# Optimization experiments

Hardware: AMD Instinct MI355X
Metric: run time of the kernel (lower is better)

The kernel has to match this reference:

```python
import jax, jax.numpy as jnp
import numpy as np

L, B, S, D, H, F, V = 6, 4, 512, 768, 12, 3072, 30522
DH = D // H
EPS = 1e-12
SCALE = 1.0 / float(np.sqrt(DH))


def _ln(x, g, b):
    m = jnp.mean(x, axis=-1, keepdims=True)
    v = jnp.mean(jnp.square(x - m), axis=-1, keepdims=True)
    return (x - m) * jax.lax.rsqrt(v + EPS) * g + b


def _mha(xq, xkv, Wq, bq, Wk, bk, Wv, bv, causal):
    Bc, Sq, _ = xq.shape
    Sk = xkv.shape[1]
    q = (xq @ Wq + bq).reshape(Bc, Sq, H, DH).transpose(0, 2, 1, 3)
    k = (xkv @ Wk + bk).reshape(Bc, Sk, H, DH).transpose(0, 2, 1, 3)
    v = (xkv @ Wv + bv).reshape(Bc, Sk, H, DH).transpose(0, 2, 1, 3)
    s = jnp.einsum('bhqd,bhkd->bhqk', q, k) * SCALE
    if causal is not None:
        s = jnp.where(causal[None, None], s, -jnp.inf)
    p = jax.nn.softmax(s, axis=-1)
    ctx = jnp.einsum('bhqk,bhkd->bhqd', p, v)
    return ctx.transpose(0, 2, 1, 3).reshape(Bc, Sq, H * DH)


def _fwd(input_ids, encoder_hidden, word_emb, pos_emb, tok_emb, emb_g, emb_b,
         Wq, bq, Wk, bk, Wv, bv, Wo, bo, ln1_g, ln1_b,
         cWq, cbq, cWk, cbk, cWv, cbv, cWo, cbo, ln2_g, ln2_b,
         Wi, bi, Wf, bf, ln3_g, ln3_b,
         Wt, bt, lnh_g, lnh_b, Wdec, bdec):
    Bc, Sc = input_ids.shape
    # BertEmbeddings: word + position + token_type(all zeros) -> LayerNorm
    h = word_emb[input_ids] + pos_emb[:Sc][None] + tok_emb[0][None, None]
    h = _ln(h, emb_g, emb_b)
    causal = jnp.tril(jnp.ones((Sc, Sc), dtype=bool))
    for l in range(L):
        # causal self-attention + residual LayerNorm
        ctx = _mha(h, h, Wq[l], bq[l], Wk[l], bk[l], Wv[l], bv[l], causal)
        h = _ln(h + ctx @ Wo[l] + bo[l], ln1_g[l], ln1_b[l])
        # cross-attention over encoder_hidden (no mask) + residual LayerNorm
        ctx = _mha(h, encoder_hidden, cWq[l], cbq[l], cWk[l], cbk[l], cWv[l], cbv[l], None)
        h = _ln(h + ctx @ cWo[l] + cbo[l], ln2_g[l], ln2_b[l])
        # FFN (erf-gelu) + residual LayerNorm
        ff = jax.nn.gelu(h @ Wi[l] + bi[l], approximate=False) @ Wf[l] + bf[l]
        h = _ln(h + ff, ln3_g[l], ln3_b[l])
    # BertOnlyMLMHead: transform (dense+gelu+LN) then vocab projection
    t = _ln(jax.nn.gelu(h @ Wt + bt, approximate=False), lnh_g, lnh_b)
    return t @ Wdec + bdec


def setup_inputs() -> dict:
    keys = iter(jax.random.split(jax.random.key(0), 64))
    def rn(shape, s=0.02):
        return jax.random.normal(next(keys), shape, jnp.float32) * s
    inp = {
        'input_ids': jax.random.randint(next(keys), (B, S), 0, V),
        'encoder_hidden': jax.random.normal(next(keys), (B, S, D), jnp.float32),
        'word_emb': rn((V, D)), 'pos_emb': rn((S, D)), 'tok_emb': rn((2, D)),
        'emb_g': jnp.ones((D,), jnp.float32), 'emb_b': jnp.zeros((D,), jnp.float32),
        'Wq': rn((L, D, D)), 'bq': jnp.zeros((L, D), jnp.float32),
        'Wk': rn((L, D, D)), 'bk': jnp.zeros((L, D), jnp.float32),
        'Wv': rn((L, D, D)), 'bv': jnp.zeros((L, D), jnp.float32),
        'Wo': rn((L, D, D)), 'bo': jnp.zeros((L, D), jnp.float32),
        'ln1_g': jnp.ones((L, D), jnp.float32), 'ln1_b': jnp.zeros((L, D), jnp.float32),
        'cWq': rn((L, D, D)), 'cbq': jnp.zeros((L, D), jnp.float32),
        'cWk': rn((L, D, D)), 'cbk': jnp.zeros((L, D), jnp.float32),
        'cWv': rn((L, D, D)), 'cbv': jnp.zeros((L, D), jnp.float32),
        'cWo': rn((L, D, D)), 'cbo': jnp.zeros((L, D), jnp.float32),
        'ln2_g': jnp.ones((L, D), jnp.float32), 'ln2_b': jnp.zeros((L, D), jnp.float32),
        'Wi': rn((L, D, F)), 'bi': jnp.zeros((L, F), jnp.float32),
        'Wf': rn((L, F, D)), 'bf': jnp.zeros((L, D), jnp.float32),
        'ln3_g': jnp.ones((L, D), jnp.float32), 'ln3_b': jnp.zeros((L, D), jnp.float32),
        'Wt': rn((D, D)), 'bt': jnp.zeros((D,), jnp.float32),
        'lnh_g': jnp.ones((D,), jnp.float32), 'lnh_b': jnp.zeros((D,), jnp.float32),
        'Wdec': rn((D, V)), 'bdec': jnp.zeros((V,), jnp.float32),
    }
    return inp


def reference(input_ids, encoder_hidden, word_emb, pos_emb, tok_emb, emb_g, emb_b,
              Wq, bq, Wk, bk, Wv, bv, Wo, bo, ln1_g, ln1_b,
              cWq, cbq, cWk, cbk, cWv, cbv, cWo, cbo, ln2_g, ln2_b,
              Wi, bi, Wf, bf, ln3_g, ln3_b,
              Wt, bt, lnh_g, lnh_b, Wdec, bdec):
    return _fwd(input_ids, encoder_hidden, word_emb, pos_emb, tok_emb, emb_g, emb_b,
                Wq, bq, Wk, bk, Wv, bv, Wo, bo, ln1_g, ln1_b,
                cWq, cbq, cWk, cbk, cWv, cbv, cWo, cbo, ln2_g, ln2_b,
                Wi, bi, Wf, bf, ln3_g, ln3_b,
                Wt, bt, lnh_g, lnh_b, Wdec, bdec)
```

## Files before the change

### kernel.cpp

```cpp
#include <hip/hip_runtime.h>
#include <math.h>

typedef unsigned short u16;
typedef unsigned int   u32;
typedef long long      i64;
typedef __attribute__((ext_vector_type(8))) __bf16 bf16x8;
typedef __attribute__((ext_vector_type(4))) float  f32x4;
typedef __attribute__((ext_vector_type(8))) u16    u16x8;
typedef __attribute__((ext_vector_type(4))) u16    u16x4;

#define LN_EPS 1e-12f

__device__ __forceinline__ float b2f(u16 u){ union {u32 i; float f;} v; v.i = ((u32)u)<<16; return v.f; }
__device__ __forceinline__ u16 f2b(float f){ union {float f; u32 i;} v; v.f = f; u32 r = v.i + 0x7FFFu + ((v.i>>16)&1u); return (u16)(r>>16); }

__device__ __forceinline__ void gl2lds16(const u16* g, u16* l) {
  __builtin_amdgcn_global_load_lds((const __attribute__((address_space(1))) void*)g,
                                   (__attribute__((address_space(3))) void*)l, 16, 0, 0);
}

struct GemmArgs {
  const u16* A; const u16* Bt; void* C;
  const float* bias0; const float* bias1; const float* bias2;
  i64 sAb, sAh, sBb, sBh, sCb, sCh;
  int lda, ldb, ldc, M, N, K, bias_seg, act, hdiv, cf32;
};

template<int BM, int BN, int WM, int WN>
__global__ __launch_bounds__(WM*WN*64)
void gemm_bt(GemmArgs g) {
  constexpr int NT = WM*WN*64;
  constexpr int RA = (BM*32)/(NT*8);
  constexpr int RB = (BN*32)/(NT*8);
  __shared__ u16 As[BM*32];
  __shared__ u16 Bs[BN*32];
  const int tid  = threadIdx.x;
  const int wave = tid >> 6, lane = tid & 63;
  const int wm = wave / WN, wn = wave % WN;
  const int z  = blockIdx.z;
  const int zb = z / g.hdiv, zh = z % g.hdiv;

  int bx, by;
  {
    const int gx = gridDim.x;
    const int nwg = gx * gridDim.y;
    const int wg = blockIdx.y * gx + blockIdx.x;
    const int q = nwg >> 3, r = nwg & 7;
    const int xcd = wg & 7, loc = wg >> 3;
    const int nid = (xcd < r ? xcd * (q + 1) : r * (q + 1) + (xcd - r) * q) + loc;
    bx = nid % gx; by = nid / gx;
  }

  const u16* A  = g.A  + (i64)zb*g.sAb + (i64)zh*g.sAh + (i64)bx*BM*g.lda;
  const u16* Bt = g.Bt + (i64)zb*g.sBb + (i64)zh*g.sBh;
  const int n0 = by * BN;
  const int lrow = lane & 15, quad = lane >> 4;

  f32x4 acc[4][4];
  #pragma unroll
  for (int i=0;i<4;i++)
    #pragma unroll
    for (int j=0;j<4;j++) acc[i][j] = (f32x4){0.f,0.f,0.f,0.f};

  for (int k0 = 0; k0 < g.K; k0 += 32) {
    #pragma unroll
    for (int r = 0; r < RA; r++) {
      int gran = r*NT + tid;
      int row = gran >> 2;
      int col = (gran & 3) << 3;
      const u16* src = A + (i64)row*g.lda + k0 + col;
      int base = (r*NT + (wave<<6)) << 3;
      gl2lds16(src, &As[base]);
    }
    #pragma unroll
    for (int r = 0; r < RB; r++) {
      int gran = r*NT + tid;
      int row = gran >> 2;
      int nrow = n0 + row; if (nrow >= g.N) nrow = g.N - 1;
      int col = (gran & 3) << 3;
      const u16* src = Bt + (i64)nrow*g.ldb + k0 + col;
      int base = (r*NT + (wave<<6)) << 3;
      gl2lds16(src, &Bs[base]);
    }
    __syncthreads();
    bf16x8 af[4], bfv[4];
    #pragma unroll
    for (int i=0;i<4;i++) af[i]  = *(const bf16x8*)&As[(((wm<<6)+(i<<4)+lrow)<<5) + (quad<<3)];
    #pragma unroll
    for (int j=0;j<4;j++) bfv[j] = *(const bf16x8*)&Bs[(((wn<<6)+(j<<4)+lrow)<<5) + (quad<<3)];
    #pragma unroll
    for (int i=0;i<4;i++)
      #pragma unroll
      for (int j=0;j<4;j++)
        acc[i][j] = __builtin_amdgcn_mfma_f32_16x16x32_bf16(af[i], bfv[j], acc[i][j], 0,0,0);
    __syncthreads();
  }

  const i64 rowbase = (i64)bx*BM + (wm<<6);
  u16*   Cb = (u16*)g.C   + (i64)zb*g.sCb + (i64)zh*g.sCh;
  float* Cf = (float*)g.C + (i64)zb*g.sCb + (i64)zh*g.sCh;
  #pragma unroll
  for (int i=0;i<4;i++) {
    #pragma unroll
    for (int j=0;j<4;j++) {
      int col = n0 + (wn<<6) + (j<<4) + lrow;
      if (col < g.N) {
        float bias = 0.f;
        if (g.bias0) {
          int seg = col / g.bias_seg;
          const float* bp = (seg==0) ? g.bias0 : ((seg==1) ? g.bias1 : g.bias2);
          bias = bp[col - seg*g.bias_seg];
        }
        #pragma unroll
        for (int r=0;r<4;r++) {
          i64 row = rowbase + (i<<4) + (quad<<2) + r;
          float v = acc[i][j][r] + bias;
          if (g.act == 1) v = 0.5f*v*(1.0f + erff(v*0.70710678118654752f));
          if (g.cf32) Cf[row*(i64)g.ldc + col] = v;
          else        Cb[row*(i64)g.ldc + col] = f2b(v);
        }
      }
    }
  }
}

__global__ __launch_bounds__(64) void flash_attn(const u16* __restrict__ qkv,
                                                 const u16* __restrict__ VT,
                                                 u16* __restrict__ ctx, int causal) {
  const int lane = threadIdx.x & 63;
  const int qi = lane & 15, g = lane >> 4;
  const int q0 = blockIdx.x << 4;
  const int bh = blockIdx.y;
  const int b = bh / 12, h = bh % 12;
  const int q = q0 + qi;

  const u16* Qp = qkv + (i64)(b*512 + q)*2304 + h*64 + (g<<3);
  bf16x8 qf0 = *(const bf16x8*)Qp;
  bf16x8 qf1 = *(const bf16x8*)(Qp + 32);

  const u16* Kp = qkv + ((i64)(b*512 + qi))*2304 + 768 + h*64 + (g<<3);
  const u16* Vp = VT + (i64)bh*32768 + (i64)qi*512 + (g<<3);

  f32x4 o[4];
  #pragma unroll
  for (int s=0;s<4;s++) o[s] = (f32x4){0.f,0.f,0.f,0.f};
  float m = -1e30f, lsum = 0.f;

  const int sA = qi + ((g & 1) << 5);
  const int sB = sA + 16;
  const int tsel = g >> 1;

  const int nt = causal ? (q0 >> 6) + 1 : 8;
  for (int kt = 0; kt < nt; ++kt) {
    const int kv0 = kt << 6;

    bf16x8 kf[4][2];
    #pragma unroll
    for (int t=0;t<4;t++)
      #pragma unroll
      for (int w=0;w<2;w++)
        kf[t][w] = *(const bf16x8*)(Kp + (i64)(kv0 + (t<<4))*2304 + (w<<5));
    bf16x8 vf[4][2];
    #pragma unroll
    for (int s=0;s<4;s++)
      #pragma unroll
      for (int w=0;w<2;w++)
        vf[s][w] = *(const bf16x8*)(Vp + (s<<13) + kv0 + (w<<5));

    f32x4 sc[4];
    #pragma unroll
    for (int t=0;t<4;t++) {
      sc[t] = (f32x4){0.f,0.f,0.f,0.f};
      sc[t] = __builtin_amdgcn_mfma_f32_16x16x32_bf16(kf[t][0], qf0, sc[t], 0,0,0);
      sc[t] = __builtin_amdgcn_mfma_f32_16x16x32_bf16(kf[t][1], qf1, sc[t], 0,0,0);
    }

    float x[4][4];
    #pragma unroll
    for (int t=0;t<4;t++)
      #pragma unroll
      for (int r=0;r<4;r++) {
        float v = sc[t][r] * 0.125f;
        int key = kv0 + (t<<4) + (g<<2) + r;
        if (causal && key > q) v = -1e30f;
        x[t][r] = v;
      }

    float mt = x[0][0];
    #pragma unroll
    for (int t=0;t<4;t++)
      #pragma unroll
      for (int r=0;r<4;r++) mt = fmaxf(mt, x[t][r]);
    mt = fmaxf(mt, __shfl_xor(mt, 16));
    mt = fmaxf(mt, __shfl_xor(mt, 32));
    float mn = fmaxf(m, mt);
    float c = __expf(m - mn);
    m = mn;

    float p[4][4];
    float ps = 0.f;
    #pragma unroll
    for (int t=0;t<4;t++)
      #pragma unroll
      for (int r=0;r<4;r++) { float e = __expf(x[t][r] - mn); p[t][r] = e; ps += e; }
    ps += __shfl_xor(ps, 16);
    ps += __shfl_xor(ps, 32);
    lsum = lsum * c + ps;
    #pragma unroll
    for (int s=0;s<4;s++) o[s] *= c;

    u32 pkLo[4], pkHi[4];
    #pragma unroll
    for (int t=0;t<4;t++) {
      pkLo[t] = (u32)f2b(p[t][0]) | ((u32)f2b(p[t][1]) << 16);
      pkHi[t] = (u32)f2b(p[t][2]) | ((u32)f2b(p[t][3]) << 16);
    }

    #pragma unroll
    for (int w=0;w<2;w++) {
      u32 w0=0, w1=0, w2=0, w3=0;
      #pragma unroll
      for (int tl=0; tl<2; ++tl) {
        const int t = 2*w + tl;
        u32 aLo = (u32)__shfl((int)pkLo[t], sA);
        u32 aHi = (u32)__shfl((int)pkHi[t], sA);
        u32 bLo = (u32)__shfl((int)pkLo[t], sB);
        u32 bHi = (u32)__shfl((int)pkHi[t], sB);
        if (tsel == tl) { w0=aLo; w1=aHi; w2=bLo; w3=bHi; }
      }
      union { bf16x8 v; u32 u[4]; } pf;
      pf.u[0]=w0; pf.u[1]=w1; pf.u[2]=w2; pf.u[3]=w3;
      #pragma unroll
      for (int s=0;s<4;s++)
        o[s] = __builtin_amdgcn_mfma_f32_16x16x32_bf16(vf[s][w], pf.v, o[s], 0,0,0);
    }
  }

  float inv = 1.0f / lsum;
  u16* orow = ctx + (i64)(b*512 + q)*768 + h*64 + (g<<2);
  #pragma unroll
  for (int s=0;s<4;s++) {
    u16x4 ov;
    #pragma unroll
    for (int r=0;r<4;r++) ov[r] = f2b(o[s][r] * inv);
    *(u16x4*)(orow + (s<<4)) = ov;
  }
}

__device__ __forceinline__ float block_reduce_sum_256(float v, float* red) {
  #pragma unroll
  for (int off=32; off; off>>=1) v += __shfl_xor(v, off);
  int wave = threadIdx.x >> 6;
  __syncthreads();
  if ((threadIdx.x & 63) == 0) red[wave] = v;
  __syncthreads();
  return red[0]+red[1]+red[2]+red[3];
}

__global__ __launch_bounds__(256) void resln_kernel(const float* base, const float* delta,
                                                    const float* gam, const float* bet,
                                                    float* out_f, u16* out_b) {
  __shared__ float red[4];
  i64 off = (i64)blockIdx.x * 768;
  int tid = threadIdx.x;
  float x[3];
  #pragma unroll
  for (int j=0;j<3;j++) {
    int i = tid + j*256;
    float v = delta[off+i];
    if (base) v += base[off+i];
    x[j] = v;
  }
  float s = block_reduce_sum_256(x[0]+x[1]+x[2], red);
  float mean = s * (1.0f/768.0f);
  float q = 0.f;
  #pragma unroll
  for (int j=0;j<3;j++) { float d = x[j]-mean; q += d*d; }
  q = block_reduce_sum_256(q, red);
  float r = rsqrtf(q*(1.0f/768.0f) + LN_EPS);
  #pragma unroll
  for (int j=0;j<3;j++) {
    int i = tid + j*256;
    float y = (x[j]-mean)*r*gam[i] + bet[i];
    out_f[off+i] = y;
    out_b[off+i] = f2b(y);
  }
}

__global__ __launch_bounds__(256) void embed_kernel(const int* ids, const float* wemb,
    const float* pemb, const float* temb, const float* gam, const float* bet,
    float* out_f, u16* out_b) {
  __shared__ float red[4];
  int row = blockIdx.x;
  int s = row & 511;
  i64 wrow = (i64)ids[row] * 768;
  i64 off = (i64)row * 768;
  int tid = threadIdx.x;
  float x[3];
  #pragma unroll
  for (int j=0;j<3;j++) {
    int i = tid + j*256;
    x[j] = wemb[wrow+i] + pemb[(i64)s*768+i] + temb[i];
  }
  float sm = block_reduce_sum_256(x[0]+x[1]+x[2], red);
  float mean = sm * (1.0f/768.0f);
  float q = 0.f;
  #pragma unroll
  for (int j=0;j<3;j++) { float d = x[j]-mean; q += d*d; }
  q = block_reduce_sum_256(q, red);
  float r = rsqrtf(q*(1.0f/768.0f) + LN_EPS);
  #pragma unroll
  for (int j=0;j<3;j++) {
    int i = tid + j*256;
    float y = (x[j]-mean)*r*gam[i] + bet[i];
    out_f[off+i] = y;
    out_b[off+i] = f2b(y);
  }
}

__global__ __launch_bounds__(256) void cvt_kernel(const float* src, u16* dst, int n) {
  int i = (blockIdx.x*256 + threadIdx.x) * 4;
  if (i + 3 < n) {
    float4 v = *(const float4*)&src[i];
    dst[i+0]=f2b(v.x); dst[i+1]=f2b(v.y); dst[i+2]=f2b(v.z); dst[i+3]=f2b(v.w);
  }
}

struct TransEntry { const float* src; u16* dst; int K, N, tile0; };
struct TransArgs  { TransEntry e[12]; int n; };

__global__ __launch_bounds__(256) void transpose_multi(TransArgs ta) {
  __shared__ u16 tile[64][72];
  int t = blockIdx.x;
  int ei = 0;
  for (int i=1;i<ta.n;i++) if (t >= ta.e[i].tile0) ei = i;
  TransEntry E = ta.e[ei];
  int lt = t - E.tile0;
  int ntn = (E.N + 63) >> 6;
  int tk = lt / ntn, tn = lt - tk*ntn;
  int tid = threadIdx.x;
  int kk = tid >> 2, c = (tid & 3) << 4;
  i64 gk = (i64)(tk*64 + kk);
  int gn0 = tn*64 + c;
  const float* srow = E.src + gk * E.N;
  if (gn0 + 16 <= E.N) {
    #pragma unroll
    for (int j=0;j<16;j++) tile[kk][c+j] = f2b(srow[gn0+j]);
  } else {
    for (int j=0;j<16;j++) tile[kk][c+j] = (gn0+j < E.N) ? f2b(srow[gn0+j]) : (u16)0;
  }
  __syncthreads();
  int nn = tid >> 2, kc = (tid & 3) << 4;
  int gn = tn*64 + nn;
  if (gn < E.N) {
    u16x8 v0, v1;
    #pragma unroll
    for (int j=0;j<8;j++) { v0[j] = tile[kc+j][nn]; v1[j] = tile[kc+8+j][nn]; }
    u16* drow = E.dst + (i64)gn*E.K + tk*64 + kc;
    *(u16x8*)&drow[0] = v0;
    *(u16x8*)&drow[8] = v1;
  }
}

__global__ __launch_bounds__(256) void vtrans_kernel(const u16* qkv, u16* VT) {
  __shared__ u16 tile[64][72];
  int bh = blockIdx.z; int b = bh / 12, hh = bh % 12;
  const u16* src = qkv + (i64)b*512*2304 + 1536 + hh*64;
  u16* dst = VT + (i64)bh*64*512;
  int kt = blockIdx.x;
  int tid = threadIdx.x;
  int kk = tid >> 2, c = (tid & 3) << 4;
  const u32* p = (const u32*)&src[(i64)(kt*64+kk)*2304 + c];
  #pragma unroll
  for (int j=0;j<8;j++) *(u32*)&tile[kk][c + 2*j] = p[j];
  __syncthreads();
  int dd = tid >> 2, kc = (tid & 3) << 4;
  u16x8 v0, v1;
  #pragma unroll
  for (int j=0;j<8;j++) { v0[j] = tile[kc+j][dd]; v1[j] = tile[kc+8+j][dd]; }
  u16* drow = dst + (i64)dd*512 + kt*64 + kc;
  *(u16x8*)&drow[0] = v0;
  *(u16x8*)&drow[8] = v1;
}

static void gemm_args(GemmArgs& g, const u16* A, int lda, const u16* Bt, int ldb,
                      void* C, int ldc, int M, int N, int K, const float* b0,
                      const float* b1, const float* b2, int bias_seg, int act, int cf32) {
  g.A=A; g.Bt=Bt; g.C=C; g.bias0=b0; g.bias1=b1; g.bias2=b2;
  g.sAb=0; g.sAh=0; g.sBb=0; g.sBh=0; g.sCb=0; g.sCh=0;
  g.lda=lda; g.ldb=ldb; g.ldc=ldc; g.M=M; g.N=N; g.K=K;
  g.bias_seg=bias_seg; g.act=act; g.hdiv=1; g.cf32=cf32;
}

static void gemm128(const u16* A, int lda, const u16* Bt, int ldb, void* C, int ldc,
                    int M, int N, int K, const float* b0, const float* b1, const float* b2,
                    int bias_seg, int act, int cf32, hipStream_t st) {
  GemmArgs g; gemm_args(g, A, lda, Bt, ldb, C, ldc, M, N, K, b0, b1, b2, bias_seg, act, cf32);
  dim3 grid(M/128, (N+127)/128, 1);
  gemm_bt<128,128,2,2><<<grid, 256, 0, st>>>(g);
}

static void gemm64(const u16* A, int lda, const u16* Bt, int ldb, void* C, int ldc,
                   int M, int N, int K, const float* b0, const float* b1, const float* b2,
                   int bias_seg, int act, int cf32, hipStream_t st) {
  GemmArgs g; gemm_args(g, A, lda, Bt, ldb, C, ldc, M, N, K, b0, b1, b2, bias_seg, act, cf32);
  dim3 grid(M/64, (N+127)/128, 1);
  gemm_bt<64,128,1,2><<<grid, 128, 0, st>>>(g);
}

extern "C" void kernel_launch(void* const* d_in, const int* in_sizes, int n_in,
                              void* d_out, int out_size, void* d_ws, size_t ws_size,
                              hipStream_t stream) {
  (void)in_sizes; (void)n_in; (void)out_size;
  const int*   ids  = (const int*)d_in[0];
  const float* enc  = (const float*)d_in[1];
  const float* wemb = (const float*)d_in[2];
  const float* pemb = (const float*)d_in[3];
  const float* temb = (const float*)d_in[4];
  const float* eg   = (const float*)d_in[5];
  const float* eb   = (const float*)d_in[6];
  const float* Wq=(const float*)d_in[7];  const float* bq=(const float*)d_in[8];
  const float* Wk=(const float*)d_in[9];  const float* bk=(const float*)d_in[10];
  const float* Wv=(const float*)d_in[11]; const float* bv=(const float*)d_in[12];
  const float* Wo=(const float*)d_in[13]; const float* bo=(const float*)d_in[14];
  const float* l1g=(const float*)d_in[15]; const float* l1b=(const float*)d_in[16];
  const float* cWq=(const float*)d_in[17]; const float* cbq=(const float*)d_in[18];
  const float* cWk=(const float*)d_in[19]; const float* cbk=(const float*)d_in[20];
  const float* cWv=(const float*)d_in[21]; const float* cbv=(const float*)d_in[22];
  const float* cWo=(const float*)d_in[23]; const float* cbo=(const float*)d_in[24];
  const float* l2g=(const float*)d_in[25]; const float* l2b=(const float*)d_in[26];
  const float* Wi=(const float*)d_in[27];  const float* bi=(const float*)d_in[28];
  const float* Wf=(const float*)d_in[29];  const float* bff=(const float*)d_in[30];
  const float* l3g=(const float*)d_in[31]; const float* l3b=(const float*)d_in[32];
  const float* Wt=(const float*)d_in[33];  const float* bt=(const float*)d_in[34];
  const float* lhg=(const float*)d_in[35]; const float* lhb=(const float*)d_in[36];
  const float* Wdec=(const float*)d_in[37]; const float* bdec=(const float*)d_in[38];
  float* out = (float*)d_out;

  u16* ws     = (u16*)d_ws;
  u16* WT     = ws;
  u16* h_bf   = WT + 24030720;
  float* h_f  = (float*)(h_bf + 1572864);
  float* h2_f = h_f + 1572864;
  u16* qkv    = (u16*)(h2_f + 1572864);
  u16* ctx    = qkv + 4718592;
  u16* VT     = ctx + 1572864;
  u16* enc_bf = VT + 1572864;
  u16* Smat   = enc_bf + 1572864;
  u16* mid    = Smat;
  if (ws_size < (size_t)53915136 * 2) return;

  const int DD = 589824, DF = 2359296;
  u16* qkvT = WT;
  u16* woT  = WT + 1769472;
  u16* cqT  = WT + 2359296;
  u16* ckvT = WT + 2949120;
  u16* cwoT = WT + 4128768;
  u16* wiT  = WT + 4718592;
  u16* wfT  = WT + 7077888;

  embed_kernel<<<2048, 256, 0, stream>>>(ids, wemb, pemb, temb, eg, eb, h_f, h_bf);
  cvt_kernel<<<1536, 256, 0, stream>>>(enc, enc_bf, 1572864);

  for (int l = 0; l < 6; l++) {
    TransArgs ta; int tile = 0; int idx = 0;
    auto add = [&](const float* s, u16* d, int K, int N) {
      ta.e[idx].src=s; ta.e[idx].dst=d; ta.e[idx].K=K; ta.e[idx].N=N; ta.e[idx].tile0=tile;
      tile += (K/64)*((N+63)/64); idx++;
    };
    add(Wq +(i64)l*DD, qkvT,        768, 768);
    add(Wk +(i64)l*DD, qkvT+DD,     768, 768);
    add(Wv +(i64)l*DD, qkvT+2*DD,   768, 768);
    add(Wo +(i64)l*DD, woT,         768, 768);
    add(cWq+(i64)l*DD, cqT,         768, 768);
    add(cWk+(i64)l*DD, ckvT,        768, 768);
    add(cWv+(i64)l*DD, ckvT+DD,     768, 768);
    add(cWo+(i64)l*DD, cwoT,        768, 768);
    add(Wi +(i64)l*DF, wiT,         768, 3072);
    add(Wf +(i64)l*DF, wfT,         3072, 768);
    ta.n = idx;
    transpose_multi<<<tile, 256, 0, stream>>>(ta);

    gemm128(h_bf, 768, qkvT, 768, qkv, 2304, 2048, 2304, 768,
            bq+l*768, bk+l*768, bv+l*768, 768, 0, 0, stream);
    vtrans_kernel<<<dim3(8,1,48), 256, 0, stream>>>(qkv, VT);
    flash_attn<<<dim3(32,48), 64, 0, stream>>>(qkv, VT, ctx, 1);
    gemm64(ctx, 768, woT, 768, h2_f, 768, 2048, 768, 768,
           bo+l*768, nullptr, nullptr, 768, 0, 1, stream);
    resln_kernel<<<2048, 256, 0, stream>>>(h_f, h2_f, l1g+l*768, l1b+l*768, h_f, h_bf);

    gemm64(h_bf, 768, cqT, 768, qkv, 2304, 2048, 768, 768,
           cbq+l*768, nullptr, nullptr, 768, 0, 0, stream);
    gemm64(enc_bf, 768, ckvT, 768, qkv+768, 2304, 2048, 1536, 768,
           cbk+l*768, cbv+l*768, nullptr, 768, 0, 0, stream);
    vtrans_kernel<<<dim3(8,1,48), 256, 0, stream>>>(qkv, VT);
    flash_attn<<<dim3(32,48), 64, 0, stream>>>(qkv, VT, ctx, 0);
    gemm64(ctx, 768, cwoT, 768, h2_f, 768, 2048, 768, 768,
           cbo+l*768, nullptr, nullptr, 768, 0, 1, stream);
    resln_kernel<<<2048, 256, 0, stream>>>(h_f, h2_f, l2g+l*768, l2b+l*768, h_f, h_bf);

    gemm128(h_bf, 768, wiT, 768, mid, 3072, 2048, 3072, 768,
            bi+l*3072, nullptr, nullptr, 3072, 1, 0, stream);
    gemm64(mid, 3072, wfT, 3072, h2_f, 768, 2048, 768, 3072,
           bff+l*768, nullptr, nullptr, 768, 0, 1, stream);
    resln_kernel<<<2048, 256, 0, stream>>>(h_f, h2_f, l3g+l*768, l3b+l*768, h_f, h_bf);
  }

  u16* wtT   = WT;
  u16* wdecT = WT + 589824;
  {
    TransArgs ta; int tile = 0; int idx = 0;
    auto add = [&](const float* s, u16* d, int K, int N) {
      ta.e[idx].src=s; ta.e[idx].dst=d; ta.e[idx].K=K; ta.e[idx].N=N; ta.e[idx].tile0=tile;
      tile += (K/64)*((N+63)/64); idx++;
    };
    add(Wt,   wtT,   768, 768);
    add(Wdec, wdecT, 768, 30522);
    ta.n = idx;
    transpose_multi<<<tile, 256, 0, stream>>>(ta);
  }
  gemm64(h_bf, 768, wtT, 768, h2_f, 768, 2048, 768, 768, bt, nullptr, nullptr, 768, 1, 1, stream);
  resln_kernel<<<2048, 256, 0, stream>>>(nullptr, h2_f, lhg, lhb, h_f, h_bf);
  gemm128(h_bf, 768, wdecT, 768, out, 30522, 2048, 30522, 768,
          bdec, nullptr, nullptr, 30522, 0, 1, stream);
}
```

Baseline: 2.672 ms.

## Double-buffer GEMM LDS tiles with XOR swizzle and larger vocab tile

Rewrites the bf16 MFMA GEMM to double-buffer its LDS tiles, issuing the next K-step's global-to-LDS loads before computing on the current one, which removes one barrier per iteration. It XOR-swizzles the LDS layout to cut bank conflicts on fragment reads. The XCD remapping now applies only to grids of at least 512 blocks, and the vocab projection uses a new 256x256, 512-thread tile configuration. The cost is double the LDS per block and more registers for the large tile, which may lower occupancy.

After: 2.532 ms. 5.2% less time.

```diff
diff --git a/kernel.cpp b/kernel.cpp
--- a/kernel.cpp
+++ b/kernel.cpp
@@ -22,88 +22,102 @@
 struct GemmArgs {
   const u16* A; const u16* Bt; void* C;
   const float* bias0; const float* bias1; const float* bias2;
-  i64 sAb, sAh, sBb, sBh, sCb, sCh;
-  int lda, ldb, ldc, M, N, K, bias_seg, act, hdiv, cf32;
+  int lda, ldb, ldc, M, N, K, bias_seg, act, cf32;
 };
 
 template<int BM, int BN, int WM, int WN>
 __global__ __launch_bounds__(WM*WN*64)
-void gemm_bt(GemmArgs g) {
-  constexpr int NT = WM*WN*64;
-  constexpr int RA = (BM*32)/(NT*8);
-  constexpr int RB = (BN*32)/(NT*8);
-  __shared__ u16 As[BM*32];
-  __shared__ u16 Bs[BN*32];
+void gemm_bt2(GemmArgs g) {
+  constexpr int NTHR = WM*WN*64;
+  constexpr int MI = BM/(WM*16);
+  constexpr int NJ = BN/(WN*16);
+  constexpr int RA = (BM*4)/NTHR;
+  constexpr int RB = (BN*4)/NTHR;
+  __shared__ u16 As[2][BM*32];
+  __shared__ u16 Bs[2][BN*32];
   const int tid  = threadIdx.x;
   const int wave = tid >> 6, lane = tid & 63;
   const int wm = wave / WN, wn = wave % WN;
-  const int z  = blockIdx.z;
-  const int zb = z / g.hdiv, zh = z % g.hdiv;
+  const int lrow = lane & 15, quad = lane >> 4;
 
   int bx, by;
   {
     const int gx = gridDim.x;
     const int nwg = gx * gridDim.y;
     const int wg = blockIdx.y * gx + blockIdx.x;
-    const int q = nwg >> 3, r = nwg & 7;
-    const int xcd = wg & 7, loc = wg >> 3;
-    const int nid = (xcd < r ? xcd * (q + 1) : r * (q + 1) + (xcd - r) * q) + loc;
-    bx = nid % gx; by = nid / gx;
-  }
-
-  const u16* A  = g.A  + (i64)zb*g.sAb + (i64)zh*g.sAh + (i64)bx*BM*g.lda;
-  const u16* Bt = g.Bt + (i64)zb*g.sBb + (i64)zh*g.sBh;
+    if (nwg >= 512) {
+      const int q = nwg >> 3, r = nwg & 7;
+      const int xcd = wg & 7, loc = wg >> 3;
+      const int nid = (xcd < r ? xcd * (q + 1) : r * (q + 1) + (xcd - r) * q) + loc;
+      bx = nid % gx; by = nid / gx;
+    } else { bx = blockIdx.x; by = blockIdx.y; }
+  }
+
+  const u16* Ab = g.A + (i64)bx*BM*g.lda;
+  const u16* Bt = g.Bt;
   const int n0 = by * BN;
-  const int lrow = lane & 15, quad = lane >> 4;
-
-  f32x4 acc[4][4];
-  #pragma unroll
-  for (int i=0;i<4;i++)
-    #pragma unroll
-    for (int j=0;j<4;j++) acc[i][j] = (f32x4){0.f,0.f,0.f,0.f};
-
-  for (int k0 = 0; k0 < g.K; k0 += 32) {
-    #pragma unroll
-    for (int r = 0; r < RA; r++) {
-      int gran = r*NT + tid;
-      int row = gran >> 2;
-      int col = (gran & 3) << 3;
-      const u16* src = A + (i64)row*g.lda + k0 + col;
-      int base = (r*NT + (wave<<6)) << 3;
-      gl2lds16(src, &As[base]);
-    }
-    #pragma unroll
-    for (int r = 0; r < RB; r++) {
-      int gran = r*NT + tid;
-      int row = gran >> 2;
-      int nrow = n0 + row; if (nrow >= g.N) nrow = g.N - 1;
-      int col = (gran & 3) << 3;
-      const u16* src = Bt + (i64)nrow*g.ldb + k0 + col;
-      int base = (r*NT + (wave<<6)) << 3;
-      gl2lds16(src, &Bs[base]);
-    }
+
+  const int srow = tid >> 2;
+  const int sps  = tid & 3;
+
+  f32x4 acc[MI][NJ];
+  #pragma unroll
+  for (int i=0;i<MI;i++)
+    #pragma unroll
+    for (int j=0;j<NJ;j++) acc[i][j] = (f32x4){0.f,0.f,0.f,0.f};
+
+  auto stage = [&](int buf, int k0) {
+    #pragma unroll
+    for (int la=0; la<RA; ++la) {
+      int row = la*(NTHR>>2) + srow;
+      int ls = sps ^ ((row>>1)&3);
+      const u16* src = Ab + (i64)row*g.lda + k0 + (ls<<3);
+      gl2lds16(src, &As[buf][(la*NTHR + (wave<<6))<<3]);
+    }
+    #pragma unroll
+    for (int la=0; la<RB; ++la) {
+      int row = la*(NTHR>>2) + srow;
+      int nrow = n0 + row; if (nrow >= g.N) nrow = g.N-1;
+      int ls = sps ^ ((row>>1)&3);
+      const u16* src = Bt + (i64)nrow*g.ldb + k0 + (ls<<3);
+      gl2lds16(src, &Bs[buf][(la*NTHR + (wave<<6))<<3]);
+    }
+  };
+
+  const int NT = g.K >> 5;
+  stage(0, 0);
+  __syncthreads();
+  for (int t = 0; t < NT; ++t) {
+    const int cur = t & 1;
+    if (t+1 < NT) stage(cur^1, (t+1)<<5);
+    const int xr = (lrow>>1)&3;
+    bf16x8 a[MI], b[NJ];
+    #pragma unroll
+    for (int i=0;i<MI;i++) {
+      int r = wm*(MI*16) + i*16 + lrow;
+      a[i] = *(const bf16x8*)&As[cur][r*32 + ((quad^xr)<<3)];
+    }
+    #pragma unroll
+    for (int j=0;j<NJ;j++) {
+      int r = wn*(NJ*16) + j*16 + lrow;
+      b[j] = *(const bf16x8*)&Bs[cur][r*32 + ((quad^xr)<<3)];
+    }
+    #pragma unroll
+    for (int i=0;i<MI;i++)
+      #pragma unroll
+      for (int j=0;j<NJ;j++)
+        acc[i][j] = __builtin_amdgcn_mfma_f32_16x16x32_bf16(a[i], b[j], acc[i][j], 0,0,0);
     __syncthreads();
-    bf16x8 af[4], bfv[4];
-    #pragma unroll
-    for (int i=0;i<4;i++) af[i]  = *(const bf16x8*)&As[(((wm<<6)+(i<<4)+lrow)<<5) + (quad<<3)];
-    #pragma unroll
-    for (int j=0;j<4;j++) bfv[j] = *(const bf16x8*)&Bs[(((wn<<6)+(j<<4)+lrow)<<5) + (quad<<3)];
-    #pragma unroll
-    for (int i=0;i<4;i++)
-      #pragma unroll
-      for (int j=0;j<4;j++)
-        acc[i][j] = __builtin_amdgcn_mfma_f32_16x16x32_bf16(af[i], bfv[j], acc[i][j], 0,0,0);
-    __syncthreads();
-  }
-
-  const i64 rowbase = (i64)bx*BM + (wm<<6);
-  u16*   Cb = (u16*)g.C   + (i64)zb*g.sCb + (i64)zh*g.sCh;
-  float* Cf = (float*)g.C + (i64)zb*g.sCb + (i64)zh*g.sCh;
-  #pragma unroll
-  for (int i=0;i<4;i++) {
-    #pragma unroll
-    for (int j=0;j<4;j++) {
-      int col = n0 + (wn<<6) + (j<<4) + lrow;
+  }
+
+  const i64 rowbase = (i64)bx*BM + wm*(MI*16);
+  u16*   Cb = (u16*)g.C;
+  float* Cf = (float*)g.C;
+  #pragma unroll
+  for (int i=0;i<MI;i++) {
+    #pragma unroll
+    for (int j=0;j<NJ;j++) {
+      int col = n0 + wn*(NJ*16) + (j<<4) + lrow;
       if (col < g.N) {
         float bias = 0.f;
         if (g.bias0) {
@@ -387,25 +401,29 @@
                       void* C, int ldc, int M, int N, int K, const float* b0,
                       const float* b1, const float* b2, int bias_seg, int act, int cf32) {
   g.A=A; g.Bt=Bt; g.C=C; g.bias0=b0; g.bias1=b1; g.bias2=b2;
-  g.sAb=0; g.sAh=0; g.sBb=0; g.sBh=0; g.sCb=0; g.sCh=0;
   g.lda=lda; g.ldb=ldb; g.ldc=ldc; g.M=M; g.N=N; g.K=K;
-  g.bias_seg=bias_seg; g.act=act; g.hdiv=1; g.cf32=cf32;
-}
-
-static void gemm128(const u16* A, int lda, const u16* Bt, int ldb, void* C, int ldc,
-                    int M, int N, int K, const float* b0, const float* b1, const float* b2,
-                    int bias_seg, int act, int cf32, hipStream_t st) {
-  GemmArgs g; gemm_args(g, A, lda, Bt, ldb, C, ldc, M, N, K, b0, b1, b2, bias_seg, act, cf32);
-  dim3 grid(M/128, (N+127)/128, 1);
-  gemm_bt<128,128,2,2><<<grid, 256, 0, st>>>(g);
-}
-
-static void gemm64(const u16* A, int lda, const u16* Bt, int ldb, void* C, int ldc,
+  g.bias_seg=bias_seg; g.act=act; g.cf32=cf32;
+}
+
+static void g2_128(const u16* A, int lda, const u16* Bt, int ldb, void* C, int ldc,
                    int M, int N, int K, const float* b0, const float* b1, const float* b2,
                    int bias_seg, int act, int cf32, hipStream_t st) {
   GemmArgs g; gemm_args(g, A, lda, Bt, ldb, C, ldc, M, N, K, b0, b1, b2, bias_seg, act, cf32);
-  dim3 grid(M/64, (N+127)/128, 1);
-  gemm_bt<64,128,1,2><<<grid, 128, 0, st>>>(g);
+  gemm_bt2<128,128,2,2><<<dim3(M/128, (N+127)/128), 256, 0, st>>>(g);
+}
+
+static void g2_64(const u16* A, int lda, const u16* Bt, int ldb, void* C, int ldc,
+                  int M, int N, int K, const float* b0, const float* b1, const float* b2,
+                  int bias_seg, int act, int cf32, hipStream_t st) {
+  GemmArgs g; gemm_args(g, A, lda, Bt, ldb, C, ldc, M, N, K, b0, b1, b2, bias_seg, act, cf32);
+  gemm_bt2<64,128,1,2><<<dim3(M/64, (N+127)/128), 128, 0, st>>>(g);
+}
+
+static void g2_256(const u16* A, int lda, const u16* Bt, int ldb, void* C, int ldc,
+                   int M, int N, int K, const float* b0, const float* b1, const float* b2,
+                   int bias_seg, int act, int cf32, hipStream_t st) {
+  GemmArgs g; gemm_args(g, A, lda, Bt, ldb, C, ldc, M, N, K, b0, b1, b2, bias_seg, act, cf32);
+  gemm_bt2<256,256,2,4><<<dim3(M/256, (N+255)/256), 512, 0, st>>>(g);
 }
 
 extern "C" void kernel_launch(void* const* d_in, const int* in_sizes, int n_in,
@@ -481,28 +499,28 @@
     ta.n = idx;
     transpose_multi<<<tile, 256, 0, stream>>>(ta);
 
-    gemm128(h_bf, 768, qkvT, 768, qkv, 2304, 2048, 2304, 768,
-            bq+l*768, bk+l*768, bv+l*768, 768, 0, 0, stream);
+    g2_128(h_bf, 768, qkvT, 768, qkv, 2304, 2048, 2304, 768,
+           bq+l*768, bk+l*768, bv+l*768, 768, 0, 0, stream);
     vtrans_kernel<<<dim3(8,1,48), 256, 0, stream>>>(qkv, VT);
     flash_attn<<<dim3(32,48), 64, 0, stream>>>(qkv, VT, ctx, 1);
-    gemm64(ctx, 768, woT, 768, h2_f, 768, 2048, 768, 768,
-           bo+l*768, nullptr, nullptr, 768, 0, 1, stream);
+    g2_64(ctx, 768, woT, 768, h2_f, 768, 2048, 768, 768,
+          bo+l*768, nullptr, nullptr, 768, 0, 1, stream);
     resln_kernel<<<2048, 256, 0, stream>>>(h_f, h2_f, l1g+l*768, l1b+l*768, h_f, h_bf);
 
-    gemm64(h_bf, 768, cqT, 768, qkv, 2304, 2048, 768, 768,
-           cbq+l*768, nullptr, nullptr, 768, 0, 0, stream);
-    gemm64(enc_bf, 768, ckvT, 768, qkv+768, 2304, 2048, 1536, 768,
-           cbk+l*768, cbv+l*768, nullptr, 768, 0, 0, stream);
+    g2_64(h_bf, 768, cqT, 768, qkv, 2304, 2048, 768, 768,
+          cbq+l*768, nullptr, nullptr, 768, 0, 0, stream);
+    g2_64(enc_bf, 768, ckvT, 768, qkv+768, 2304, 2048, 1536, 768,
+          cbk+l*768, cbv+l*768, nullptr, 768, 0, 0, stream);
     vtrans_kernel<<<dim3(8,1,48), 256, 0, stream>>>(qkv, VT);
     flash_attn<<<dim3(32,48), 64, 0, stream>>>(qkv, VT, ctx, 0);
-    gemm64(ctx, 768, cwoT, 768, h2_f, 768, 2048, 768, 768,
-           cbo+l*768, nullptr, nullptr, 768, 0, 1, stream);
+    g2_64(ctx, 768, cwoT, 768, h2_f, 768, 2048, 768, 768,
+          cbo+l*768, nullptr, nullptr, 768, 0, 1, stream);
     resln_kernel<<<2048, 256, 0, stream>>>(h_f, h2_f, l2g+l*768, l2b+l*768, h_f, h_bf);
 
-    gemm128(h_bf, 768, wiT, 768, mid, 3072, 2048, 3072, 768,
-            bi+l*3072, nullptr, nullptr, 3072, 1, 0, stream);
-    gemm64(mid, 3072, wfT, 3072, h2_f, 768, 2048, 768, 3072,
-           bff+l*768, nullptr, nullptr, 768, 0, 1, stream);
+    g2_128(h_bf, 768, wiT, 768, mid, 3072, 2048, 3072, 768,
+           bi+l*3072, nullptr, nullptr, 3072, 1, 0, stream);
+    g2_64(mid, 3072, wfT, 3072, h2_f, 768, 2048, 768, 3072,
+          bff+l*768, nullptr, nullptr, 768, 0, 1, stream);
     resln_kernel<<<2048, 256, 0, stream>>>(h_f, h2_f, l3g+l*768, l3b+l*768, h_f, h_bf);
   }
 
@@ -519,8 +537,8 @@
     ta.n = idx;
     transpose_multi<<<tile, 256, 0, stream>>>(ta);
   }
-  gemm64(h_bf, 768, wtT, 768, h2_f, 768, 2048, 768, 768, bt, nullptr, nullptr, 768, 1, 1, stream);
+  g2_64(h_bf, 768, wtT, 768, h2_f, 768, 2048, 768, 768, bt, nullptr, nullptr, 768, 1, 1, stream);
   resln_kernel<<<2048, 256, 0, stream>>>(nullptr, h2_f, lhg, lhb, h_f, h_bf);
-  gemm128(h_bf, 768, wdecT, 768, out, 30522, 2048, 30522, 768,
-          bdec, nullptr, nullptr, 30522, 0, 1, stream);
-}
+  g2_256(h_bf, 768, wdecT, 768, out, 30522, 2048, 30522, 768,
+         bdec, nullptr, nullptr, 30522, 0, 1, stream);
+}
```
